# Optimization experiments

Measured on AMD Instinct MI355X. Metric: run time of the kernel, lower is better.

## Reference

```python
import jax, jax.numpy as jnp
import numpy as np

B, S, D, DOM, L = 16, 512, 512, 8, 3  # batch, seq_len, mem_dim (S==D required by outputs*rel), domains, layers


def setup_inputs() -> dict:
    key = jax.random.key(0)
    ks = jax.random.split(key, 16)
    adj = jax.random.uniform(ks[0], (B, S, S), jnp.float32)
    rel = jax.random.uniform(ks[1], (B, S, S), jnp.float32)
    gcn_inputs = jax.random.normal(ks[2], (B, S, D), jnp.float32)
    frontrel = jax.random.normal(ks[3], (B, S, D), jnp.float32)
    backrel = jax.random.normal(ks[4], (B, S, D), jnp.float32)
    # depmap: exactly one selected column per (b, row) so masked_select reshapes to [B,S]
    depmap = jax.nn.one_hot(jax.random.randint(ks[5], (B, S), 0, S), S, dtype=jnp.float32)
    dom_idx = jax.random.randint(ks[6], (B, S), 0, DOM)
    has_dom = jax.random.bernoulli(ks[7], 0.5, (B, S)).astype(jnp.float32)
    domain_id = jax.nn.one_hot(dom_idx, DOM, dtype=jnp.float32) * has_dom[..., None]
    redom_idx = jax.random.randint(ks[8], (B, S), 0, DOM)
    has_re = jax.random.bernoulli(ks[9], 0.5, (B, S)).astype(jnp.float32)
    redomain_id = jax.nn.one_hot(redom_idx, DOM, dtype=jnp.float32) * has_re[..., None]
    domain = jax.random.bernoulli(ks[10], 0.5, (B, S, DOM, 1))
    mask = jnp.ones((B, S), dtype=bool)
    sc = 1.0 / np.sqrt(D)
    W_layers = jax.random.normal(ks[11], (L, D, D), jnp.float32) * sc
    b_layers = jnp.zeros((L, D), jnp.float32)
    prelu_a = jnp.full((L,), 0.25, jnp.float32)  # nn.PReLU default
    W_dg = jax.random.normal(ks[12], (D, D), jnp.float32) * sc
    b_dg = jnp.zeros((D,), jnp.float32)
    W_mg = jax.random.normal(ks[13], (2 * D, D), jnp.float32) * (1.0 / np.sqrt(2 * D))
    b_mg = jnp.zeros((D,), jnp.float32)
    W_out = jax.random.normal(ks[14], (L * D, D), jnp.float32) * (1.0 / np.sqrt(L * D))
    b_out = jnp.zeros((D,), jnp.float32)
    return dict(adj=adj, domain=domain, domain_id=domain_id, redomain_id=redomain_id,
                frontrel=frontrel, backrel=backrel, depmap=depmap, rel=rel,
                gcn_inputs=gcn_inputs, mask=mask, W_layers=W_layers, b_layers=b_layers,
                prelu_a=prelu_a, W_dg=W_dg, b_dg=b_dg, W_mg=W_mg, b_mg=b_mg,
                W_out=W_out, b_out=b_out)


def _forward(adj, domain, domain_id, redomain_id, frontrel, backrel, depmap, rel,
             gcn_inputs, W_layers, b_layers, prelu_a, W_dg, b_dg, W_mg, b_mg, W_out, b_out):
    denom = jnp.sum(adj, axis=2, keepdims=True) + 1.0                     # [B,S,1]
    domain_mask = jnp.sum(domain_id, axis=-1, keepdims=True) == 1.0       # [B,S,1]
    redomain_mask = jnp.sum(redomain_id, axis=-1, keepdims=True) == 1.0   # [B,S,1]
    frontadj = jnp.sum(adj * depmap, axis=-1)                             # [B,S]
    backadj = jnp.sum(jnp.swapaxes(adj, -1, -2) * depmap, axis=-1)        # [B,S]
    outputs = gcn_inputs
    outs = []
    for l in range(L):
        frontoutputs = jnp.where(domain_mask, 0.0, outputs)
        backoutputs = jnp.where(redomain_mask, 0.0, jnp.einsum('bij,bjd->bid', rel, outputs))
        # domain pooling: mask then max over sequence -> [B,DOM,D]
        pooled = jnp.max(jnp.where(domain, -10000.0, outputs[:, :, None, :]), axis=1)
        domain_outputs = jax.nn.sigmoid(pooled @ W_dg + b_dg)             # domain_gate
        frontoutputs = frontoutputs + jnp.einsum('bsk,bkd->bsd', domain_id, domain_outputs)
        backoutputs = backoutputs + jnp.einsum('bsk,bkd->bsd', redomain_id, domain_outputs)
        frontdepadj = jax.nn.sigmoid(jnp.concatenate([frontoutputs, frontrel], -1) @ W_mg + b_mg)
        backdepadj = jax.nn.sigmoid(jnp.concatenate([backoutputs, backrel], -1) @ W_mg + b_mg)
        delta = jnp.einsum('bji,bjd->bid', rel, frontadj[..., None] * frontdepadj * frontoutputs)
        delta = delta + backadj[..., None] * backdepadj * backoutputs
        Ax = jnp.einsum('bij,bjd->bid', adj, outputs * rel)               # requires S==D
        AxW = (Ax @ W_layers[l] + b_layers[l]) + (outputs @ W_layers[l] + b_layers[l]) + delta
        x = AxW / denom
        outputs = jnp.where(x >= 0, x, prelu_a[l] * x)                    # PReLU
        outs.append(outputs)                                              # dropout is eval-mode identity
    gcn_outputs = jnp.concatenate(outs, axis=2)                           # [B,S,L*D]
    return gcn_outputs @ W_out + b_out + gcn_inputs


def reference(adj, domain, domain_id, redomain_id, frontrel, backrel, depmap, rel,
              gcn_inputs, mask, W_layers, b_layers, prelu_a, W_dg, b_dg, W_mg, b_mg,
              W_out, b_out):
    return _forward(adj, domain, domain_id, redomain_id, frontrel, backrel, depmap, rel,
                    gcn_inputs, W_layers, b_layers, prelu_a, W_dg, b_dg, W_mg, b_mg,
                    W_out, b_out)
```

## Files before the change

kernel.cpp:

```cpp
#include <hip/hip_runtime.h>
#include <math.h>

#define SD_  (512*512)
#define BSD_ (16*512*512)

typedef unsigned short u16;
typedef short s16x8 __attribute__((ext_vector_type(8)));
typedef float f32x4 __attribute__((ext_vector_type(4)));

__device__ __forceinline__ float sigmoidf_(float x) { return 1.0f / (1.0f + __expf(-x)); }

__device__ __forceinline__ u16 f2bf(float f) {
    unsigned int u = __float_as_uint(f);
    u += 0x7fffu + ((u >> 16) & 1u);
    return (u16)(u >> 16);
}
__device__ __forceinline__ float bf2f(u16 h) { return __uint_as_float((unsigned)h << 16); }

__device__ __forceinline__ void glds16(const void* g, void* l) {
    __builtin_amdgcn_global_load_lds((const __attribute__((address_space(1))) unsigned int*)g,
                                     (__attribute__((address_space(3))) unsigned int*)l, 16, 0, 0);
}

struct GP {
    const u16 *A1, *A2;  int lda1, lda2;  long sA;
    const u16 *B1, *B2;  int ldb1, ldb2;  long sB;
    void *C1, *C2;  int obf1, obf2, ldc1, ldc2;  long sC;
    u16 *CT1, *CT2;  long sCT;
    const void *Ci1, *Ci2;  int cm1, cm2, ldci1, ldci2;  long sCi1, sCi2;
    const float *bias;  float bS;
    const float *sc1, *sc2;
    const int *selm1, *seli1, *selm2, *seli2;
    const u16 *DG;
    const float *invden, *prelu;  int pidx;
    int M, K, zs, swzX, swzY;
};

template<int EPI, int ASEL>
__global__ __launch_bounds__(512, 4)
void gemm3(const GP p)
{
    __shared__ short LS[32768];
    const int tid = threadIdx.x;
    int bx, by, bz;
    if (p.swzX >= 0) {
        const int bid = blockIdx.x + gridDim.x * (blockIdx.y + gridDim.y * blockIdx.z);
        const int ppx = (gridDim.y * gridDim.z) >> 3;
        const int xcd = bid & 7, idx = bid >> 3;
        const int pair = xcd * ppx + (idx >> p.swzX);
        bx = idx & ((1 << p.swzX) - 1);
        by = pair & ((1 << p.swzY) - 1);
        bz = pair >> p.swzY;
    } else { bx = blockIdx.x; by = blockIdx.y; bz = blockIdx.z; }

    const int seg = (bz >= p.zs) ? 1 : 0;
    const int z = seg ? bz - p.zs : bz;
    const u16* Ab = (seg ? p.A2 : p.A1) + z * p.sA;
    const int lda = seg ? p.lda2 : p.lda1;
    const u16* Bb = (seg ? p.B2 : p.B1) + z * p.sB;
    const int ldb = seg ? p.ldb2 : p.ldb1;

    const int m0 = by * 128, n0 = bx * 128;
    const int srow = ((tid >> 6) << 4) | (tid & 15);
    const int sk0 = ((tid >> 4) & 3) << 3;
    const int slot = ((srow >> 4) << 9) + (sk0 << 4) + ((srow & 15) << 3);

    const u16* aRow = Ab + (long)(m0 + srow) * lda + sk0;
    if (ASEL) {
        const int* selm = seg ? p.selm2 : p.selm1;
        const int* seli = seg ? p.seli2 : p.seli1;
        const int r0 = m0 + srow;
        if (selm[r0]) aRow = p.DG + (long)(((r0 >> 9) << 3) + seli[r0]) * 512 + sk0;
    }
    const u16* bRow = Bb + (long)(n0 + srow) * ldb + sk0;

    auto stage = [&](int kb2) {
        short* base = &LS[(kb2 & 1) * 16384];
        const int kk = kb2 << 6;
        glds16(aRow + kk,      &base[slot]);
        glds16(aRow + kk + 32, &base[4096 + slot]);
        glds16(bRow + kk,      &base[8192 + slot]);
        glds16(bRow + kk + 32, &base[12288 + slot]);
    };

    const int wave = tid >> 6, lane = tid & 63;
    const int gA = (wave >> 2) << 2;
    const int gB = (wave & 3) << 1;

    f32x4 acc[4][2] = {};
    const int nkb = p.K >> 6;

    stage(0);
    for (int kb = 0; kb < nkb; ++kb) {
        if (kb + 1 < nkb) {
            stage(kb + 1);
            asm volatile("s_waitcnt vmcnt(4)" ::: "memory");
        } else {
            asm volatile("s_waitcnt vmcnt(0)" ::: "memory");
        }
        __builtin_amdgcn_s_barrier();
        const short* ls = &LS[(kb & 1) * 16384];
#pragma unroll
        for (int kh = 0; kh < 2; ++kh) {
            s16x8 aF[4], bF[2];
#pragma unroll
            for (int mt = 0; mt < 4; ++mt) aF[mt] = *(const s16x8*)&ls[kh * 4096 + ((gA + mt) * 64 + lane) * 8];
#pragma unroll
            for (int nt = 0; nt < 2; ++nt) bF[nt] = *(const s16x8*)&ls[8192 + kh * 4096 + ((gB + nt) * 64 + lane) * 8];
#pragma unroll
            for (int mt = 0; mt < 4; ++mt)
#pragma unroll
                for (int nt = 0; nt < 2; ++nt)
                    acc[mt][nt] = __builtin_amdgcn_mfma_f32_16x16x32_bf16(aF[mt], bF[nt], acc[mt][nt], 0, 0, 0);
        }
        __builtin_amdgcn_s_barrier();
    }

    const int ml = lane & 15, quad = lane >> 4;
    const int wm = (wave >> 2) * 64, wn = (wave & 3) * 32;
    u16* Cb16 = (u16*)(seg ? p.C2 : p.C1);
    float* Cb32 = (float*)(seg ? p.C2 : p.C1);
    const int haveC = (seg ? p.C2 : p.C1) != nullptr;
    const int obf = seg ? p.obf2 : p.obf1;
    const int ldc = seg ? p.ldc2 : p.ldc1;
    if (haveC) { if (obf) Cb16 += z * p.sC; else Cb32 += z * p.sC; }
    u16* CTb = seg ? p.CT2 : p.CT1;
    if (CTb) CTb += z * p.sCT;
    const u16* CiT = (const u16*)(seg ? p.Ci2 : p.Ci1);
    const float* Ci32 = (const float*)(seg ? p.Ci2 : p.Ci1);
    const int cm = seg ? p.cm2 : p.cm1;
    const int ldci = seg ? p.ldci2 : p.ldci1;
    {
        const long sCi = seg ? p.sCi2 : p.sCi1;
        if (cm) CiT += z * sCi; else Ci32 += z * sCi;
    }
    const float pal = (EPI == 4) ? p.prelu[p.pidx] : 0.0f;
    const float* scp = (EPI == 8) ? (seg ? p.sc2 : p.sc1) : nullptr;
    const int* eselm = (EPI == 8) ? (seg ? p.selm2 : p.selm1) : nullptr;
    const int* eseli2 = (EPI == 8) ? (seg ? p.seli2 : p.seli1) : nullptr;

    const bool useEp = haveC && (obf == 1);
    u16* Lds = (u16*)LS;
    const int bb = m0 >> 9, ss = m0 & 511;
    const int cd = tid >> 2, cso = (tid & 3) * 32;

    float cinAll[8][4];
    if (EPI == 3 || EPI == 4 || EPI == 7 || EPI == 8) {
        if (cm) {
            __syncthreads();
            const u16* srcc = CiT + (long)bb * SD_ + (long)(n0 + cd) * 512 + ss + cso;
            u16* dstc = &Lds[cd * 136 + cso];
#pragma unroll
            for (int j = 0; j < 4; ++j) *(s16x8*)&dstc[j * 8] = *(const s16x8*)&srcc[j * 8];
            __syncthreads();
#pragma unroll
            for (int mt = 0; mt < 4; ++mt)
#pragma unroll
                for (int nt = 0; nt < 2; ++nt) {
                    const ushort4 c4 = *(const ushort4*)&Lds[(wn + nt * 16 + ml) * 136 + wm + mt * 16 + quad * 4];
                    cinAll[mt * 2 + nt][0] = bf2f(c4.x); cinAll[mt * 2 + nt][1] = bf2f(c4.y);
                    cinAll[mt * 2 + nt][2] = bf2f(c4.z); cinAll[mt * 2 + nt][3] = bf2f(c4.w);
                }
        } else {
#pragma unroll
            for (int mt = 0; mt < 4; ++mt)
#pragma unroll
                for (int nt = 0; nt < 2; ++nt) {
                    const int col = n0 + wn + nt * 16 + ml;
                    const int rowb = m0 + wm + mt * 16 + quad * 4;
#pragma unroll
                    for (int r = 0; r < 4; ++r) cinAll[mt * 2 + nt][r] = Ci32[(long)(rowb + r) * ldci + col];
                }
        }
    }

    u16 pkAll[8][4];
#pragma unroll
    for (int mt = 0; mt < 4; ++mt) {
#pragma unroll
        for (int nt = 0; nt < 2; ++nt) {
            const int col = n0 + wn + nt * 16 + ml;
            const int rowb = m0 + wm + mt * 16 + quad * 4;
#pragma unroll
            for (int r = 0; r < 4; ++r) {
                const int row = rowb + r;
                float x = acc[mt][nt][r];
                if (EPI == 1) x += p.bias[col];
                else if (EPI == 3) x += cinAll[mt * 2 + nt][r];
                else if (EPI == 4) {
                    x = (x + p.bS * p.bias[col] + cinAll[mt * 2 + nt][r]) * p.invden[z * p.M + row];
                    x = (x >= 0.0f) ? x : pal * x;
                }
                else if (EPI == 6) x = sigmoidf_(x + p.bias[col]);
                else if (EPI == 7) x += p.bias[col] + cinAll[mt * 2 + nt][r];
                else if (EPI == 8) {
                    float av;
                    if (eselm[row]) av = bf2f(p.DG[(long)(((row >> 9) << 3) + eseli2[row]) * 512 + col]);
                    else av = bf2f(Ab[(long)row * lda + col]);
                    x = sigmoidf_(x + cinAll[mt * 2 + nt][r]) * scp[row] * av;
                }
                if (haveC && obf == 0) Cb32[(long)row * ldc + col] = x;
                pkAll[mt * 2 + nt][r] = f2bf(x);
            }
        }
    }

    if (CTb) {
        __syncthreads();
#pragma unroll
        for (int mt = 0; mt < 4; ++mt)
#pragma unroll
            for (int nt = 0; nt < 2; ++nt)
                *(ushort4*)&Lds[(wn + nt * 16 + ml) * 136 + wm + mt * 16 + quad * 4] =
                    *(const ushort4*)&pkAll[mt * 2 + nt][0];
        __syncthreads();
        u16* dstt = CTb + (long)bb * SD_ + (long)(n0 + cd) * 512 + ss + cso;
#pragma unroll
        for (int j = 0; j < 4; ++j) *(s16x8*)&dstt[j * 8] = *(const s16x8*)&Lds[cd * 136 + cso + j * 8];
    }

    if (useEp) {
        __syncthreads();
#pragma unroll
        for (int mt = 0; mt < 4; ++mt)
#pragma unroll
            for (int nt = 0; nt < 2; ++nt)
#pragma unroll
                for (int r = 0; r < 4; ++r)
                    Lds[(wm + mt * 16 + quad * 4 + r) * 136 + wn + nt * 16 + ml] = pkAll[mt * 2 + nt][r];
        __syncthreads();
#pragma unroll
        for (int j = 0; j < 4; ++j) {
            const s16x8 v = *(const s16x8*)&Lds[cd * 136 + cso + j * 8];
            *(s16x8*)&Cb16[(long)(m0 + cd) * ldc + n0 + cso + j * 8] = v;
        }
    }
}

__global__ __launch_bounds__(256)
void cvt_k(const float* __restrict__ s, u16* __restrict__ d)
{
    const long i = ((long)blockIdx.x * 256 + threadIdx.x) * 4;
    const float4 v = *(const float4*)&s[i];
    ushort4 h = { f2bf(v.x), f2bf(v.y), f2bf(v.z), f2bf(v.w) };
    *(ushort4*)&d[i] = h;
}

__global__ __launch_bounds__(256)
void trcvt_k(const float* __restrict__ src, u16* __restrict__ dstT, u16* __restrict__ dstN,
             const int R, const int C, const long sS, const long sDT, const long sDN)
{
    __shared__ u16 t[64][72];
    const float* s = src + blockIdx.z * sS;
    const int r0 = blockIdx.y * 64, c0 = blockIdx.x * 64;
    const int tid = threadIdx.x;
    const int lr = tid >> 2, lc4 = (tid & 3) * 16;
#pragma unroll
    for (int j = 0; j < 4; ++j) {
        const float4 v = *(const float4*)&s[(long)(r0 + lr) * C + c0 + lc4 + j * 4];
        ushort4 h = { f2bf(v.x), f2bf(v.y), f2bf(v.z), f2bf(v.w) };
        *(ushort4*)&t[lr][lc4 + j * 4] = h;
        if (dstN) *(ushort4*)&dstN[blockIdx.z * sDN + (long)(r0 + lr) * C + c0 + lc4 + j * 4] = h;
    }
    __syncthreads();
    const int lcol = tid >> 2, rc = (tid & 3) * 16;
#pragma unroll
    for (int j = 0; j < 2; ++j) {
        s16x8 v;
#pragma unroll
        for (int q = 0; q < 8; ++q) v[q] = (short)t[rc + j * 8 + q][lcol];
        *(s16x8*)&dstT[blockIdx.z * sDT + (long)(c0 + lcol) * R + r0 + rc + j * 8] = v;
    }
}

__global__ __launch_bounds__(256)
void e0_k(const float* __restrict__ adj, const float* __restrict__ depmap,
          const float* __restrict__ domain_id, const float* __restrict__ redomain_id,
          float* __restrict__ invden, float* __restrict__ fa, int* __restrict__ dcol,
          int* __restrict__ dm, int* __restrict__ dsel, int* __restrict__ rm, int* __restrict__ rsel)
{
    const int bs = blockIdx.x;
    const int t = threadIdx.x;
    const float* arow = adj + (long)bs * 512;
    const float* drow = depmap + (long)bs * 512;
    __shared__ float red[256];
    __shared__ int scol;
    if (t == 0) scol = 0;
    const float a0 = arow[t], a1 = arow[t + 256];
    const float p0 = drow[t], p1 = drow[t + 256];
    if (p0 > 0.5f) scol = t;
    if (p1 > 0.5f) scol = t + 256;
    red[t] = a0 + a1;
    __syncthreads();
    for (int off = 128; off > 0; off >>= 1) { if (t < off) red[t] += red[t + off]; __syncthreads(); }
    if (t == 0) invden[bs] = 1.0f / (red[0] + 1.0f);
    __syncthreads();
    red[t] = a0 * p0 + a1 * p1;
    __syncthreads();
    for (int off = 128; off > 0; off >>= 1) { if (t < off) red[t] += red[t + off]; __syncthreads(); }
    if (t == 0) {
        fa[bs] = red[0];
        dcol[bs] = scol;
        const float* q = domain_id + (long)bs * 8;
        float s = 0.f; int sel = 0;
        for (int k = 0; k < 8; ++k) { float v = q[k]; s += v; if (v > 0.5f) sel = k; }
        dm[bs] = (s > 0.5f) ? 1 : 0; dsel[bs] = sel;
        const float* r = redomain_id + (long)bs * 8;
        s = 0.f; sel = 0;
        for (int k = 0; k < 8; ++k) { float v = r[k]; s += v; if (v > 0.5f) sel = k; }
        rm[bs] = (s > 0.5f) ? 1 : 0; rsel[bs] = sel;
    }
}

__global__ void e0b_k(const float* __restrict__ adj, const int* __restrict__ dcol, float* __restrict__ ba)
{
    const int bs = blockIdx.x * 256 + threadIdx.x;
    const int b = bs >> 9, s = bs & 511;
    ba[bs] = adj[((long)b * 512 + dcol[bs]) * 512 + s];
}

__global__ __launch_bounds__(256)
void pool1_k(const u16* __restrict__ OUT, const int ldO, const int* __restrict__ domain,
             const u16* __restrict__ relb, u16* __restrict__ cm, u16* __restrict__ OxRT)
{
    const int b = blockIdx.x >> 4, c = blockIdx.x & 15;
    const int s0 = c * 32, tid = threadIdx.x;
    __shared__ int dom[256];
    dom[tid] = domain[((long)(b * 512 + s0 + (tid >> 3))) * 8 + (tid & 7)];
    __syncthreads();
    const int d0 = tid * 2;
    float mxa[8], mxb[8];
#pragma unroll
    for (int k = 0; k < 8; ++k) { mxa[k] = -10000.0f; mxb[k] = -10000.0f; }
    s16x8 pA[4], pB[4];
#pragma unroll
    for (int s = 0; s < 32; ++s) {
        const int row = b * 512 + s0 + s;
        const unsigned uv = *(const unsigned*)&OUT[(long)row * ldO + d0];
        const unsigned rv = *(const unsigned*)&relb[(long)row * 512 + d0];
        const float vx = bf2f((u16)(uv & 0xffff)), vy = bf2f((u16)(uv >> 16));
        const float rx = bf2f((u16)(rv & 0xffff)), ry = bf2f((u16)(rv >> 16));
        pA[s >> 3][s & 7] = (short)f2bf(vx * rx);
        pB[s >> 3][s & 7] = (short)f2bf(vy * ry);
        const int* ds = &dom[s * 8];
#pragma unroll
        for (int k = 0; k < 8; ++k) {
            mxa[k] = fmaxf(mxa[k], ds[k] ? -10000.0f : vx);
            mxb[k] = fmaxf(mxb[k], ds[k] ? -10000.0f : vy);
        }
    }
#pragma unroll
    for (int j = 0; j < 4; ++j) *(s16x8*)&OxRT[((long)b * 512 + d0) * 512 + s0 + j * 8] = pA[j];
#pragma unroll
    for (int j = 0; j < 4; ++j) *(s16x8*)&OxRT[((long)b * 512 + d0 + 1) * 512 + s0 + j * 8] = pB[j];
#pragma unroll
    for (int k = 0; k < 8; ++k) {
        ushort2 h = { f2bf(mxa[k]), f2bf(mxb[k]) };
        *(ushort2*)&cm[((long)((b * 16 + c) * 8 + k)) * 512 + d0] = h;
    }
}

__global__ void pool2_k(const u16* __restrict__ cm, u16* __restrict__ pooled)
{
    const int q = blockIdx.x * 256 + threadIdx.x;
    const int b = q >> 12, k = (q >> 9) & 7, d = q & 511;
    float m = -1e30f;
    for (int c = 0; c < 16; ++c)
        m = fmaxf(m, bf2f(cm[((long)((b * 16 + c) * 8 + k)) * 512 + d]));
    pooled[((long)(b * 8 + k)) * 512 + d] = f2bf(m);
}

extern "C" void kernel_launch(void* const* d_in, const int* in_sizes, int n_in,
                              void* d_out, int out_size, void* d_ws, size_t ws_size,
                              hipStream_t stream)
{
    const float* adj         = (const float*)d_in[0];
    const int*   domain      = (const int*)d_in[1];
    const float* domain_id   = (const float*)d_in[2];
    const float* redomain_id = (const float*)d_in[3];
    const float* frontrel    = (const float*)d_in[4];
    const float* backrel     = (const float*)d_in[5];
    const float* depmap      = (const float*)d_in[6];
    const float* rel         = (const float*)d_in[7];
    const float* gcn         = (const float*)d_in[8];
    const float* W_layers    = (const float*)d_in[10];
    const float* b_layers    = (const float*)d_in[11];
    const float* prelu_a     = (const float*)d_in[12];
    const float* W_dg        = (const float*)d_in[13];
    const float* b_dg        = (const float*)d_in[14];
    const float* W_mg        = (const float*)d_in[15];
    const float* b_mg        = (const float*)d_in[16];
    const float* W_out       = (const float*)d_in[17];
    const float* b_out       = (const float*)d_in[18];
    float* out = (float*)d_out;

    char* w = (char*)d_ws;
    auto alloc = [&](size_t bytes) { void* p = (void*)w; w += (bytes + 255) & ~(size_t)255; return p; };
    const size_t Bb = (size_t)BSD_ * 2;
    u16* OUTS_bf = (u16*)alloc((size_t)8192 * 1536 * 2);
    u16* OUTT    = (u16*)alloc(Bb);
    u16* gcnT    = (u16*)alloc(Bb);
    u16* RB_bf   = (u16*)alloc(Bb);
    u16* XBT     = (u16*)alloc(Bb);
    u16* XFT     = (u16*)alloc(Bb);
    u16* OxRT    = (u16*)alloc(Bb);
    u16* DLT     = (u16*)alloc(Bb);
    u16* AXO_bf  = (u16*)alloc(Bb);
    u16* BBT     = (u16*)alloc(Bb);
    u16* FBT     = (u16*)alloc(Bb);
    u16* rel_bf  = (u16*)alloc(Bb);
    u16* relT_bf = (u16*)alloc(Bb);
    u16* adj_bf  = (u16*)alloc(Bb);
    u16* gcn_bf  = (u16*)alloc(Bb);
    u16* frel_bf = (u16*)alloc(Bb);
    u16* brel_bf = (u16*)alloc(Bb);
    u16* WmgT1 = (u16*)alloc((size_t)SD_ * 2);
    u16* WmgT2 = (u16*)alloc((size_t)SD_ * 2);
    u16* WdgT  = (u16*)alloc((size_t)SD_ * 2);
    u16* WlT   = (u16*)alloc((size_t)3 * SD_ * 2);
    u16* WoutT = (u16*)alloc((size_t)512 * 1536 * 2);
    u16* cm     = (u16*)alloc((size_t)16 * 16 * 8 * 512 * 2);
    u16* pooled = (u16*)alloc((size_t)16 * 8 * 512 * 2);
    u16* DGb    = (u16*)alloc((size_t)16 * 8 * 512 * 2);
    float* invden = (float*)alloc(8192 * 4);
    float* fa     = (float*)alloc(8192 * 4);
    float* ba     = (float*)alloc(8192 * 4);
    int* dcol = (int*)alloc(8192 * 4);
    int* dm   = (int*)alloc(8192 * 4);
    int* dsel = (int*)alloc(8192 * 4);
    int* rm   = (int*)alloc(8192 * 4);
    int* rsel = (int*)alloc(8192 * 4);

    cvt_k<<<4096, 256, 0, stream>>>(adj, adj_bf);
    cvt_k<<<4096, 256, 0, stream>>>(frontrel, frel_bf);
    cvt_k<<<4096, 256, 0, stream>>>(backrel, brel_bf);
    trcvt_k<<<dim3(8, 8, 16), 256, 0, stream>>>(gcn, gcnT, gcn_bf, 512, 512, SD_, SD_, SD_);
    trcvt_k<<<dim3(8, 8, 16), 256, 0, stream>>>(rel, relT_bf, rel_bf, 512, 512, SD_, SD_, SD_);
    trcvt_k<<<dim3(8, 8, 1), 256, 0, stream>>>(W_mg, WmgT1, nullptr, 512, 512, 0, 0, 0);
    trcvt_k<<<dim3(8, 8, 1), 256, 0, stream>>>(W_mg + SD_, WmgT2, nullptr, 512, 512, 0, 0, 0);
    trcvt_k<<<dim3(8, 8, 1), 256, 0, stream>>>(W_dg, WdgT, nullptr, 512, 512, 0, 0, 0);
    trcvt_k<<<dim3(8, 8, 3), 256, 0, stream>>>(W_layers, WlT, nullptr, 512, 512, SD_, SD_, 0);
    trcvt_k<<<dim3(8, 24, 1), 256, 0, stream>>>(W_out, WoutT, nullptr, 1536, 512, 0, 0, 0);
    e0_k<<<8192, 256, 0, stream>>>(adj, depmap, domain_id, redomain_id, invden, fa, dcol, dm, dsel, rm, rsel);
    e0b_k<<<32, 256, 0, stream>>>(adj, dcol, ba);

    const dim3 blk(512);

    {
        GP p{};
        p.A1 = brel_bf; p.A2 = frel_bf; p.lda1 = p.lda2 = 512; p.sA = 0;
        p.B1 = p.B2 = WmgT2; p.ldb1 = p.ldb2 = 512; p.sB = 0;
        p.CT1 = BBT; p.CT2 = FBT; p.sCT = 0;
        p.bias = b_mg; p.M = 8192; p.K = 512; p.zs = 1; p.swzX = 2; p.swzY = 6;
        gemm3<1, 0><<<dim3(4, 64, 2), blk, 0, stream>>>(p);
    }

    for (int l = 0; l < 3; ++l) {
        const u16* OUTp  = (l == 0) ? gcn_bf : (OUTS_bf + (l - 1) * 512);
        const u16* OUTTp = (l == 0) ? gcnT : OUTT;
        const int ldO = (l == 0) ? 512 : 1536;

        {
            GP p{};
            p.A1 = rel_bf; p.lda1 = 512; p.sA = SD_;
            p.B1 = OUTTp; p.ldb1 = 512; p.sB = SD_;
            p.C1 = RB_bf; p.obf1 = 1; p.ldc1 = 512; p.sC = SD_;
            p.M = 512; p.K = 512; p.zs = 16; p.swzX = 2; p.swzY = 2;
            gemm3<0, 0><<<dim3(4, 4, 16), blk, 0, stream>>>(p);
        }
        pool1_k<<<256, 256, 0, stream>>>(OUTp, ldO, domain, rel_bf, cm, OxRT);
        pool2_k<<<256, 256, 0, stream>>>(cm, pooled);
        {
            GP p{};
            p.A1 = pooled; p.lda1 = 512; p.B1 = WdgT; p.ldb1 = 512;
            p.C1 = DGb; p.obf1 = 1; p.ldc1 = 512;
            p.bias = b_dg; p.M = 128; p.K = 512; p.zs = 1; p.swzX = -1;
            gemm3<6, 0><<<dim3(4, 1, 1), blk, 0, stream>>>(p);
        }
        {
            GP p{};
            p.A1 = RB_bf; p.lda1 = 512; p.A2 = OUTp; p.lda2 = ldO; p.sA = 0;
            p.selm1 = rm; p.seli1 = rsel; p.selm2 = dm; p.seli2 = dsel; p.DG = DGb;
            p.B1 = p.B2 = WmgT1; p.ldb1 = p.ldb2 = 512; p.sB = 0;
            p.Ci1 = BBT; p.Ci2 = FBT; p.cm1 = p.cm2 = 1; p.ldci1 = p.ldci2 = 512; p.sCi1 = p.sCi2 = 0;
            p.CT1 = XBT; p.CT2 = XFT; p.sCT = 0;
            p.sc1 = ba; p.sc2 = fa; p.M = 8192; p.K = 512; p.zs = 1; p.swzX = 2; p.swzY = 6;
            gemm3<8, 1><<<dim3(4, 64, 2), blk, 0, stream>>>(p);
        }
        {
            GP p{};
            p.A1 = relT_bf; p.lda1 = 512; p.A2 = adj_bf; p.lda2 = 512; p.sA = SD_;
            p.B1 = XFT; p.ldb1 = 512;
            p.B2 = OxRT; p.ldb2 = 512; p.sB = SD_;
            p.Ci1 = XBT; p.cm1 = 1; p.ldci1 = 512; p.sCi1 = SD_;
            p.Ci2 = OUTTp; p.cm2 = 1; p.ldci2 = 512; p.sCi2 = SD_;
            p.CT1 = DLT; p.sCT = SD_;
            p.C2 = AXO_bf; p.obf2 = 1; p.ldc2 = 512; p.sC = SD_;
            p.M = 512; p.K = 512; p.zs = 16; p.swzX = 2; p.swzY = 2;
            gemm3<3, 0><<<dim3(4, 4, 32), blk, 0, stream>>>(p);
        }
        {
            GP p{};
            p.A1 = AXO_bf; p.lda1 = 512; p.sA = SD_;
            p.B1 = WlT + (long)l * SD_; p.ldb1 = 512; p.sB = 0;
            p.Ci1 = DLT; p.cm1 = 1; p.ldci1 = 512; p.sCi1 = SD_;
            p.C1 = OUTS_bf + l * 512; p.obf1 = 1; p.ldc1 = 1536; p.sC = (long)512 * 1536;
            p.CT1 = OUTT; p.sCT = SD_;
            p.bias = b_layers + l * 512; p.bS = 2.0f;
            p.invden = invden; p.prelu = prelu_a; p.pidx = l;
            p.M = 512; p.K = 512; p.zs = 16; p.swzX = 2; p.swzY = 2;
            gemm3<4, 0><<<dim3(4, 4, 16), blk, 0, stream>>>(p);
        }
    }

    {
        GP p{};
        p.A1 = OUTS_bf; p.lda1 = 1536; p.sA = 0;
        p.B1 = WoutT; p.ldb1 = 1536; p.sB = 0;
        p.Ci1 = gcn; p.cm1 = 0; p.ldci1 = 512; p.sCi1 = 0;
        p.C1 = out; p.obf1 = 0; p.ldc1 = 512; p.sC = 0;
        p.bias = b_out; p.M = 8192; p.K = 1536; p.zs = 1; p.swzX = 2; p.swzY = 6;
        gemm3<7, 0><<<dim3(4, 64, 1), blk, 0, stream>>>(p);
    }
}
```

Measured before the change: 639.7 us.

## Add 128x64 tile variant for small GEMMs, stage fp32 residual via LDS, fuse casts

Templates the GEMM on the N tile width and adds a 128x64 variant with its own B staging, wave layout and epilogue strides. The 256-block batched GEMMs (RB, the layer-weight GEMM, domain gate) now launch twice as many blocks to fill more CUs. The final GEMM's fp32 residual input is now staged through LDS for coalesced reads, and the three fp32-to-bf16 conversion launches are merged into one kernel. The narrower tile costs more A reloads and more complex indexing.

```diff
diff --git a/kernel.cpp b/kernel.cpp
--- a/kernel.cpp
+++ b/kernel.cpp
@@ -36,11 +36,14 @@
     int M, K, zs, swzX, swzY;
 };
 
-template<int EPI, int ASEL>
+template<int EPI, int ASEL, int TN>
 __global__ __launch_bounds__(512, 4)
 void gemm3(const GP p)
 {
-    __shared__ short LS[32768];
+    __shared__ short LS[(TN == 128) ? 32768 : 24576];
+    constexpr int BUFS = (TN == 128) ? 16384 : 12288;
+    constexpr int BKH  = (TN == 128) ? 4096 : 2048;
+    constexpr int MW   = (TN == 128) ? 4 : 2;
     const int tid = threadIdx.x;
     int bx, by, bz;
     if (p.swzX >= 0) {
@@ -60,10 +63,13 @@
     const u16* Bb = (seg ? p.B2 : p.B1) + z * p.sB;
     const int ldb = seg ? p.ldb2 : p.ldb1;
 
-    const int m0 = by * 128, n0 = bx * 128;
+    const int m0 = by * 128, n0 = bx * TN;
     const int srow = ((tid >> 6) << 4) | (tid & 15);
     const int sk0 = ((tid >> 4) & 3) << 3;
     const int slot = ((srow >> 4) << 9) + (sk0 << 4) + ((srow & 15) << 3);
+    const int srB = (((tid >> 6) & 3) << 4) | (tid & 15);
+    const int skB = ((((tid >> 4) & 3) << 3) | ((tid >> 8) << 5));
+    const int bslot = (tid & 255) * 8 + (tid >> 8) * 2048;
 
     const u16* aRow = Ab + (long)(m0 + srow) * lda + sk0;
     if (ASEL) {
@@ -72,43 +78,49 @@
         const int r0 = m0 + srow;
         if (selm[r0]) aRow = p.DG + (long)(((r0 >> 9) << 3) + seli[r0]) * 512 + sk0;
     }
-    const u16* bRow = Bb + (long)(n0 + srow) * ldb + sk0;
+    const u16* bRow = (TN == 128) ? (Bb + (long)(n0 + srow) * ldb + sk0)
+                                  : (Bb + (long)(n0 + srB) * ldb + skB);
 
     auto stage = [&](int kb2) {
-        short* base = &LS[(kb2 & 1) * 16384];
+        short* base = &LS[(kb2 & 1) * BUFS];
         const int kk = kb2 << 6;
         glds16(aRow + kk,      &base[slot]);
         glds16(aRow + kk + 32, &base[4096 + slot]);
-        glds16(bRow + kk,      &base[8192 + slot]);
-        glds16(bRow + kk + 32, &base[12288 + slot]);
+        if (TN == 128) {
+            glds16(bRow + kk,      &base[8192 + slot]);
+            glds16(bRow + kk + 32, &base[12288 + slot]);
+        } else {
+            glds16(bRow + kk, &base[8192 + bslot]);
+        }
     };
 
     const int wave = tid >> 6, lane = tid & 63;
-    const int gA = (wave >> 2) << 2;
-    const int gB = (wave & 3) << 1;
-
-    f32x4 acc[4][2] = {};
+    const int gA = (TN == 128) ? ((wave >> 2) << 2) : ((wave >> 1) << 1);
+    const int gB = (TN == 128) ? ((wave & 3) << 1) : ((wave & 1) << 1);
+
+    f32x4 acc[MW][2] = {};
     const int nkb = p.K >> 6;
 
     stage(0);
     for (int kb = 0; kb < nkb; ++kb) {
         if (kb + 1 < nkb) {
             stage(kb + 1);
-            asm volatile("s_waitcnt vmcnt(4)" ::: "memory");
+            if (TN == 128) asm volatile("s_waitcnt vmcnt(4)" ::: "memory");
+            else           asm volatile("s_waitcnt vmcnt(3)" ::: "memory");
         } else {
             asm volatile("s_waitcnt vmcnt(0)" ::: "memory");
         }
         __builtin_amdgcn_s_barrier();
-        const short* ls = &LS[(kb & 1) * 16384];
+        const short* ls = &LS[(kb & 1) * BUFS];
 #pragma unroll
         for (int kh = 0; kh < 2; ++kh) {
-            s16x8 aF[4], bF[2];
-#pragma unroll
-            for (int mt = 0; mt < 4; ++mt) aF[mt] = *(const s16x8*)&ls[kh * 4096 + ((gA + mt) * 64 + lane) * 8];
-#pragma unroll
-            for (int nt = 0; nt < 2; ++nt) bF[nt] = *(const s16x8*)&ls[8192 + kh * 4096 + ((gB + nt) * 64 + lane) * 8];
-#pragma unroll
-            for (int mt = 0; mt < 4; ++mt)
+            s16x8 aF[MW], bF[2];
+#pragma unroll
+            for (int mt = 0; mt < MW; ++mt) aF[mt] = *(const s16x8*)&ls[kh * 4096 + ((gA + mt) * 64 + lane) * 8];
+#pragma unroll
+            for (int nt = 0; nt < 2; ++nt) bF[nt] = *(const s16x8*)&ls[8192 + kh * BKH + ((gB + nt) * 64 + lane) * 8];
+#pragma unroll
+            for (int mt = 0; mt < MW; ++mt)
 #pragma unroll
                 for (int nt = 0; nt < 2; ++nt)
                     acc[mt][nt] = __builtin_amdgcn_mfma_f32_16x16x32_bf16(aF[mt], bF[nt], acc[mt][nt], 0, 0, 0);
@@ -117,7 +129,8 @@
     }
 
     const int ml = lane & 15, quad = lane >> 4;
-    const int wm = (wave >> 2) * 64, wn = (wave & 3) * 32;
+    const int wm = (TN == 128) ? ((wave >> 2) * 64) : ((wave >> 1) * 32);
+    const int wn = (TN == 128) ? ((wave & 3) * 32) : ((wave & 1) * 32);
     u16* Cb16 = (u16*)(seg ? p.C2 : p.C1);
     float* Cb32 = (float*)(seg ? p.C2 : p.C1);
     const int haveC = (seg ? p.C2 : p.C1) != nullptr;
@@ -142,28 +155,53 @@
     const bool useEp = haveC && (obf == 1);
     u16* Lds = (u16*)LS;
     const int bb = m0 >> 9, ss = m0 & 511;
-    const int cd = tid >> 2, cso = (tid & 3) * 32;
-
-    float cinAll[8][4];
+    const int cd  = (TN == 128) ? (tid >> 2) : (tid >> 3);
+    const int cso = (TN == 128) ? ((tid & 3) * 32) : ((tid & 7) * 16);
+    constexpr int CJ = (TN == 128) ? 4 : 2;
+
+    float cinAll[MW * 2][4];
     if (EPI == 3 || EPI == 4 || EPI == 7 || EPI == 8) {
         if (cm) {
             __syncthreads();
             const u16* srcc = CiT + (long)bb * SD_ + (long)(n0 + cd) * 512 + ss + cso;
             u16* dstc = &Lds[cd * 136 + cso];
 #pragma unroll
-            for (int j = 0; j < 4; ++j) *(s16x8*)&dstc[j * 8] = *(const s16x8*)&srcc[j * 8];
+            for (int j = 0; j < CJ; ++j) *(s16x8*)&dstc[j * 8] = *(const s16x8*)&srcc[j * 8];
             __syncthreads();
 #pragma unroll
-            for (int mt = 0; mt < 4; ++mt)
+            for (int mt = 0; mt < MW; ++mt)
 #pragma unroll
                 for (int nt = 0; nt < 2; ++nt) {
                     const ushort4 c4 = *(const ushort4*)&Lds[(wn + nt * 16 + ml) * 136 + wm + mt * 16 + quad * 4];
                     cinAll[mt * 2 + nt][0] = bf2f(c4.x); cinAll[mt * 2 + nt][1] = bf2f(c4.y);
                     cinAll[mt * 2 + nt][2] = bf2f(c4.z); cinAll[mt * 2 + nt][3] = bf2f(c4.w);
                 }
+        } else if (EPI == 7 && TN == 128) {
+            float* Lf = (float*)LS;
+            const int lr = tid >> 2, lc = (tid & 3) * 16;
+#pragma unroll
+            for (int h = 0; h < 2; ++h) {
+                __syncthreads();
+                const float* src = Ci32 + (long)(m0 + lr) * ldci + n0 + h * 64 + lc;
+                float* dst = &Lf[lr * 68 + lc];
+#pragma unroll
+                for (int j = 0; j < 4; ++j) *(float4*)&dst[j * 4] = *(const float4*)&src[j * 4];
+                __syncthreads();
+#pragma unroll
+                for (int mt = 0; mt < MW; ++mt)
+#pragma unroll
+                    for (int nt = 0; nt < 2; ++nt) {
+                        const int colL = wn + nt * 16 + ml;
+                        if ((colL >> 6) == h) {
+#pragma unroll
+                            for (int r = 0; r < 4; ++r)
+                                cinAll[mt * 2 + nt][r] = Lf[(wm + mt * 16 + quad * 4 + r) * 68 + (colL & 63)];
+                        }
+                    }
+            }
         } else {
 #pragma unroll
-            for (int mt = 0; mt < 4; ++mt)
+            for (int mt = 0; mt < MW; ++mt)
 #pragma unroll
                 for (int nt = 0; nt < 2; ++nt) {
                     const int col = n0 + wn + nt * 16 + ml;
@@ -174,9 +212,9 @@
         }
     }
 
-    u16 pkAll[8][4];
-#pragma unroll
-    for (int mt = 0; mt < 4; ++mt) {
+    u16 pkAll[MW * 2][4];
+#pragma unroll
+    for (int mt = 0; mt < MW; ++mt) {
 #pragma unroll
         for (int nt = 0; nt < 2; ++nt) {
             const int col = n0 + wn + nt * 16 + ml;
@@ -208,7 +246,7 @@
     if (CTb) {
         __syncthreads();
 #pragma unroll
-        for (int mt = 0; mt < 4; ++mt)
+        for (int mt = 0; mt < MW; ++mt)
 #pragma unroll
             for (int nt = 0; nt < 2; ++nt)
                 *(ushort4*)&Lds[(wn + nt * 16 + ml) * 136 + wm + mt * 16 + quad * 4] =
@@ -216,31 +254,37 @@
         __syncthreads();
         u16* dstt = CTb + (long)bb * SD_ + (long)(n0 + cd) * 512 + ss + cso;
 #pragma unroll
-        for (int j = 0; j < 4; ++j) *(s16x8*)&dstt[j * 8] = *(const s16x8*)&Lds[cd * 136 + cso + j * 8];
+        for (int j = 0; j < CJ; ++j) *(s16x8*)&dstt[j * 8] = *(const s16x8*)&Lds[cd * 136 + cso + j * 8];
     }
 
     if (useEp) {
+        constexpr int LDC2 = (TN == 128) ? 136 : 72;
         __syncthreads();
 #pragma unroll
-        for (int mt = 0; mt < 4; ++mt)
+        for (int mt = 0; mt < MW; ++mt)
 #pragma unroll
             for (int nt = 0; nt < 2; ++nt)
 #pragma unroll
                 for (int r = 0; r < 4; ++r)
-                    Lds[(wm + mt * 16 + quad * 4 + r) * 136 + wn + nt * 16 + ml] = pkAll[mt * 2 + nt][r];
+                    Lds[(wm + mt * 16 + quad * 4 + r) * LDC2 + wn + nt * 16 + ml] = pkAll[mt * 2 + nt][r];
         __syncthreads();
-#pragma unroll
-        for (int j = 0; j < 4; ++j) {
-            const s16x8 v = *(const s16x8*)&Lds[cd * 136 + cso + j * 8];
-            *(s16x8*)&Cb16[(long)(m0 + cd) * ldc + n0 + cso + j * 8] = v;
+        const int cd2 = tid >> 2, cso2 = (tid & 3) * (TN == 128 ? 32 : 16);
+#pragma unroll
+        for (int j = 0; j < CJ; ++j) {
+            const s16x8 v = *(const s16x8*)&Lds[cd2 * LDC2 + cso2 + j * 8];
+            *(s16x8*)&Cb16[(long)(m0 + cd2) * ldc + n0 + cso2 + j * 8] = v;
         }
     }
 }
 
 __global__ __launch_bounds__(256)
-void cvt_k(const float* __restrict__ s, u16* __restrict__ d)
-{
-    const long i = ((long)blockIdx.x * 256 + threadIdx.x) * 4;
+void cvt3_k(const float* __restrict__ s0, const float* __restrict__ s1, const float* __restrict__ s2,
+            u16* __restrict__ d0, u16* __restrict__ d1, u16* __restrict__ d2)
+{
+    const int g = blockIdx.x >> 12;
+    const float* s = (g == 0) ? s0 : (g == 1) ? s1 : s2;
+    u16* d = (g == 0) ? d0 : (g == 1) ? d1 : d2;
+    const long i = ((long)(blockIdx.x & 4095) * 256 + threadIdx.x) * 4;
     const float4 v = *(const float4*)&s[i];
     ushort4 h = { f2bf(v.x), f2bf(v.y), f2bf(v.z), f2bf(v.w) };
     *(ushort4*)&d[i] = h;
@@ -431,9 +475,7 @@
     int* rm   = (int*)alloc(8192 * 4);
     int* rsel = (int*)alloc(8192 * 4);
 
-    cvt_k<<<4096, 256, 0, stream>>>(adj, adj_bf);
-    cvt_k<<<4096, 256, 0, stream>>>(frontrel, frel_bf);
-    cvt_k<<<4096, 256, 0, stream>>>(backrel, brel_bf);
+    cvt3_k<<<12288, 256, 0, stream>>>(adj, frontrel, backrel, adj_bf, frel_bf, brel_bf);
     trcvt_k<<<dim3(8, 8, 16), 256, 0, stream>>>(gcn, gcnT, gcn_bf, 512, 512, SD_, SD_, SD_);
     trcvt_k<<<dim3(8, 8, 16), 256, 0, stream>>>(rel, relT_bf, rel_bf, 512, 512, SD_, SD_, SD_);
     trcvt_k<<<dim3(8, 8, 1), 256, 0, stream>>>(W_mg, WmgT1, nullptr, 512, 512, 0, 0, 0);
@@ -452,7 +494,7 @@
         p.B1 = p.B2 = WmgT2; p.ldb1 = p.ldb2 = 512; p.sB = 0;
         p.CT1 = BBT; p.CT2 = FBT; p.sCT = 0;
         p.bias = b_mg; p.M = 8192; p.K = 512; p.zs = 1; p.swzX = 2; p.swzY = 6;
-        gemm3<1, 0><<<dim3(4, 64, 2), blk, 0, stream>>>(p);
+        gemm3<1, 0, 128><<<dim3(4, 64, 2), blk, 0, stream>>>(p);
     }
 
     for (int l = 0; l < 3; ++l) {
@@ -465,8 +507,8 @@
             p.A1 = rel_bf; p.lda1 = 512; p.sA = SD_;
             p.B1 = OUTTp; p.ldb1 = 512; p.sB = SD_;
             p.C1 = RB_bf; p.obf1 = 1; p.ldc1 = 512; p.sC = SD_;
-            p.M = 512; p.K = 512; p.zs = 16; p.swzX = 2; p.swzY = 2;
-            gemm3<0, 0><<<dim3(4, 4, 16), blk, 0, stream>>>(p);
+            p.M = 512; p.K = 512; p.zs = 16; p.swzX = 3; p.swzY = 2;
+            gemm3<0, 0, 64><<<dim3(8, 4, 16), blk, 0, stream>>>(p);
         }
         pool1_k<<<256, 256, 0, stream>>>(OUTp, ldO, domain, rel_bf, cm, OxRT);
         pool2_k<<<256, 256, 0, stream>>>(cm, pooled);
@@ -475,7 +517,7 @@
             p.A1 = pooled; p.lda1 = 512; p.B1 = WdgT; p.ldb1 = 512;
             p.C1 = DGb; p.obf1 = 1; p.ldc1 = 512;
             p.bias = b_dg; p.M = 128; p.K = 512; p.zs = 1; p.swzX = -1;
-            gemm3<6, 0><<<dim3(4, 1, 1), blk, 0, stream>>>(p);
+            gemm3<6, 0, 64><<<dim3(8, 1, 1), blk, 0, stream>>>(p);
         }
         {
             GP p{};
@@ -485,7 +527,7 @@
             p.Ci1 = BBT; p.Ci2 = FBT; p.cm1 = p.cm2 = 1; p.ldci1 = p.ldci2 = 512; p.sCi1 = p.sCi2 = 0;
             p.CT1 = XBT; p.CT2 = XFT; p.sCT = 0;
             p.sc1 = ba; p.sc2 = fa; p.M = 8192; p.K = 512; p.zs = 1; p.swzX = 2; p.swzY = 6;
-            gemm3<8, 1><<<dim3(4, 64, 2), blk, 0, stream>>>(p);
+            gemm3<8, 1, 128><<<dim3(4, 64, 2), blk, 0, stream>>>(p);
         }
         {
             GP p{};
@@ -497,7 +539,7 @@
             p.CT1 = DLT; p.sCT = SD_;
             p.C2 = AXO_bf; p.obf2 = 1; p.ldc2 = 512; p.sC = SD_;
             p.M = 512; p.K = 512; p.zs = 16; p.swzX = 2; p.swzY = 2;
-            gemm3<3, 0><<<dim3(4, 4, 32), blk, 0, stream>>>(p);
+            gemm3<3, 0, 128><<<dim3(4, 4, 32), blk, 0, stream>>>(p);
         }
         {
             GP p{};
@@ -508,8 +550,8 @@
             p.CT1 = OUTT; p.sCT = SD_;
             p.bias = b_layers + l * 512; p.bS = 2.0f;
             p.invden = invden; p.prelu = prelu_a; p.pidx = l;
-            p.M = 512; p.K = 512; p.zs = 16; p.swzX = 2; p.swzY = 2;
-            gemm3<4, 0><<<dim3(4, 4, 16), blk, 0, stream>>>(p);
+            p.M = 512; p.K = 512; p.zs = 16; p.swzX = 3; p.swzY = 2;
+            gemm3<4, 0, 64><<<dim3(8, 4, 16), blk, 0, stream>>>(p);
         }
     }
 
@@ -520,6 +562,6 @@
         p.Ci1 = gcn; p.cm1 = 0; p.ldci1 = 512; p.sCi1 = 0;
         p.C1 = out; p.obf1 = 0; p.ldc1 = 512; p.sC = 0;
         p.bias = b_out; p.M = 8192; p.K = 1536; p.zs = 1; p.swzX = 2; p.swzY = 6;
-        gemm3<7, 0><<<dim3(4, 64, 1), blk, 0, stream>>>(p);
-    }
-}
+        gemm3<7, 0, 128><<<dim3(4, 64, 1), blk, 0, stream>>>(p);
+    }
+}
```

New measurement: 624.2 us. -2.4%, faster.
